# Kernel optimization log

Hardware: AMD Instinct MI355X
Metric: run time of the kernel (lower is better)

## Reference

```python
import jax, jax.numpy as jnp
import numpy as np

B = 4
IN_DIM = 512
HID = 1024
MLP_LAYERS = 2
SEQ = 4096          # output_dim / sequence_length
RH = 64             # ripl_hidden_dim
RL = 2              # ripl_num_layers
MULT = 1            # ripl_coordinate_multipler

MID_DIM = 2 * RH * RH + (RH + 1) * RH      # per middle ripple layer param count
OUT_DIM = 2 * RH * 1 + (RH + 1) * 1        # output ripple layer param count
MLP_OUT = RL * MID_DIM + OUT_DIM


def gelu(x):
    return jax.nn.gelu(x, approximate=False)


def layer_norm(x, g, b, eps=1e-5):
    mu = jnp.mean(x, axis=-1, keepdims=True)
    var = jnp.var(x, axis=-1, keepdims=True)
    return (x - mu) * jax.lax.rsqrt(var + eps) * g + b


def batch_ripple(x, w, b):
    # x: (B,S,I), w: (B,O,I,2), b: (B,O,I+1)
    # out[b,s,o] = b[b,o,0] + sum_i b[b,o,i+1] * sin(w[b,o,i,0]*x[b,s,i] + w[b,o,i,1])
    arg = w[:, None, :, :, 0] * x[:, :, None, :] + w[:, None, :, :, 1]  # (B,S,O,I)
    return b[:, None, :, 0] + jnp.sum(jnp.sin(arg) * b[:, None, :, 1:], axis=-1)


def setup_inputs() -> dict:
    key = jax.random.key(0)
    ks = jax.random.split(key, 20)
    s = 0.02
    inp = {
        "x": jax.random.normal(ks[0], (B, IN_DIM), jnp.float32),
        "mlp_w0": jax.random.normal(ks[1], (IN_DIM, HID), jnp.float32) * s,
        "mlp_b0": jnp.zeros((HID,), jnp.float32),
        "mlp_w1": jax.random.normal(ks[2], (HID, HID), jnp.float32) * s,
        "mlp_b1": jnp.zeros((HID,), jnp.float32),
        "ln_g1": jnp.ones((HID,), jnp.float32),
        "ln_b1": jnp.zeros((HID,), jnp.float32),
        "mlp_w2": jax.random.normal(ks[3], (HID, HID), jnp.float32) * s,
        "mlp_b2": jnp.zeros((HID,), jnp.float32),
        "ln_g2": jnp.ones((HID,), jnp.float32),
        "ln_b2": jnp.zeros((HID,), jnp.float32),
        "mlp_w3": jax.random.normal(ks[4], (HID, MLP_OUT), jnp.float32) * s,
        "mlp_b3": jnp.zeros((MLP_OUT,), jnp.float32),
        "lc_w": jax.random.normal(ks[5], (1, RH), jnp.float32) * 0.1,
        "lc_b": jax.random.normal(ks[6], (RH,), jnp.float32) * 0.1,
        "byp_w": jax.random.normal(ks[7], (1, 1, 2), jnp.float32),
        "byp_b": jax.random.normal(ks[8], (1, 2), jnp.float32),
    }
    return inp


def reference(x, mlp_w0, mlp_b0, mlp_w1, mlp_b1, ln_g1, ln_b1,
              mlp_w2, mlp_b2, ln_g2, ln_b2, mlp_w3, mlp_b3,
              lc_w, lc_b, byp_w, byp_b):
    # hypernetwork MLP: Linear+GELU, [Linear+LN+GELU]*2, Linear
    h = gelu(x @ mlp_w0 + mlp_b0)
    h = gelu(layer_norm(h @ mlp_w1 + mlp_b1, ln_g1, ln_b1))
    h = gelu(layer_norm(h @ mlp_w2 + mlp_b2, ln_g2, ln_b2))
    mlp_out = h @ mlp_w3 + mlp_b3                      # (B, MLP_OUT)

    # split into RL middle ripple layers then the output layer
    middles = [mlp_out[:, i * MID_DIM:(i + 1) * MID_DIM] for i in range(RL)]
    out_w = mlp_out[:, RL * MID_DIM:RL * MID_DIM + OUT_DIM]

    # line coordinates -> fc layer
    lc = (jnp.arange(SEQ, dtype=jnp.float32) * MULT)[None, :, None]  # (1,S,1)
    lc = jnp.broadcast_to(lc, (x.shape[0], SEQ, 1))
    lc_x = lc @ lc_w + lc_b                                          # (B,S,RH)
    lc_bypass = lc_x

    for mw in middles:
        w = mw[:, :2 * RH * RH].reshape(-1, RH, RH, 2)
        b = mw[:, 2 * RH * RH:].reshape(-1, RH, RH + 1)
        lc_x = gelu(batch_ripple(lc_x, w, b))

    wo = out_w[:, :2 * RH].reshape(-1, 1, RH, 2)
    bo = out_w[:, 2 * RH:].reshape(-1, 1, RH + 1)
    lc_x = batch_ripple(lc_x, wo, bo)                                # (B,S,1)

    # learned RippleLinear(1,1) bypass, broadcast over features then reduced
    byp = byp_b[0, 0] + jnp.sum(
        jnp.sin(byp_w[0, 0, 0] * lc_bypass + byp_w[0, 0, 1]) * byp_b[0, 1],
        axis=-1, keepdims=True)
    lc_x = lc_x + byp
    return jnp.transpose(lc_x, (0, 2, 1))                            # (B,1,S)
```

## Files before the change

kernel.cpp:

```cpp
#include <hip/hip_runtime.h>
#include <hip/hip_bf16.h>
#include <math.h>

#define B_      4
#define IN_DIM  512
#define HID     1024
#define SEQ     4096
#define RH      64
#define RL      2
#define MID_DIM 12352
#define OUT_DIM 193
#define MLP_OUT 24897
#define INV2PI  0.15915494309189535f

#define MLPT_STRIDE 25088

#define OFF_P0    0
#define OFF_P1    32768
#define OFF_H1    98304
#define OFF_P2    102400
#define OFF_H2    167936
#define OFF_P3    172032
#define OFF_MLPT  968736

__device__ __forceinline__ float gelu_exact(float v) {
    return 0.5f * v * (1.0f + erff(v * 0.70710678118654752f));
}

__device__ __forceinline__ float hw_sin_rev(float r) {
    r = r - __builtin_rintf(r);
    return __builtin_amdgcn_sinf(r);
}

__global__ void k_gemm0(const float* __restrict__ x, const float* __restrict__ w0,
                        float* __restrict__ p0) {
    const int cch = blockIdx.x;
    const int kc  = blockIdx.y;
    const int tid = threadIdx.x;
    __shared__ float xs[256];
    {
        const int b = tid >> 6, k = tid & 63;
        xs[tid] = x[b * IN_DIM + kc * 64 + k];
    }
    __syncthreads();
    const int b = tid >> 6, cl = tid & 63;
    const int c = cch * 64 + cl;
    const float* wp = w0 + (size_t)(kc * 64) * HID + c;
    const float* xp = xs + b * 64;
    float acc = 0.f;
    #pragma unroll 8
    for (int k = 0; k < 64; ++k)
        acc = fmaf(xp[k], wp[(size_t)k * HID], acc);
    p0[(kc * 4 + b) * HID + c] = acc;
}

__global__ void k_gemm1(const float* __restrict__ p0, const float* __restrict__ b0,
                        const float* __restrict__ w1, float* __restrict__ p1) {
    const int cch = blockIdx.x;
    const int kc  = blockIdx.y;
    const int tid = threadIdx.x;
    __shared__ float hs[256];
    {
        const int b = tid >> 6, k = tid & 63;
        const int kg = kc * 64 + k;
        float v = b0[kg];
        #pragma unroll
        for (int j = 0; j < 8; ++j) v += p0[(j * 4 + b) * HID + kg];
        hs[tid] = gelu_exact(v);
    }
    __syncthreads();
    const int b = tid >> 6, cl = tid & 63;
    const int c = cch * 64 + cl;
    const float* wp = w1 + (size_t)(kc * 64) * HID + c;
    const float* hp = hs + b * 64;
    float acc = 0.f;
    #pragma unroll 8
    for (int k = 0; k < 64; ++k)
        acc = fmaf(hp[k], wp[(size_t)k * HID], acc);
    p1[(kc * 4 + b) * HID + c] = acc;
}

__global__ void k_gemm2(const float* __restrict__ h, const float* __restrict__ w,
                        float* __restrict__ pout) {
    const int cch = blockIdx.x;
    const int kc  = blockIdx.y;
    const int tid = threadIdx.x;
    __shared__ float hs[256];
    {
        const int b = tid >> 6, k = tid & 63;
        hs[tid] = h[b * HID + kc * 64 + k];
    }
    __syncthreads();
    const int b = tid >> 6, cl = tid & 63;
    const int c = cch * 64 + cl;
    const float* wp = w + (size_t)(kc * 64) * HID + c;
    const float* hp = hs + b * 64;
    float acc = 0.f;
    #pragma unroll 8
    for (int k = 0; k < 64; ++k)
        acc = fmaf(hp[k], wp[(size_t)k * HID], acc);
    pout[(kc * 4 + b) * HID + c] = acc;
}

__global__ void k_lng(const float* __restrict__ part, const float* __restrict__ bias,
                      const float* __restrict__ g, const float* __restrict__ bl,
                      float* __restrict__ h) {
    const int b = blockIdx.x, tid = threadIdx.x;
    float v = bias[tid];
    #pragma unroll
    for (int j = 0; j < 16; ++j) v += part[(j * 4 + b) * HID + tid];
    float s1 = v, s2 = v * v;
    #pragma unroll
    for (int m = 1; m < 64; m <<= 1) {
        s1 += __shfl_xor(s1, m, 64);
        s2 += __shfl_xor(s2, m, 64);
    }
    __shared__ float r1[16], r2[16], s_mu, s_rs;
    const int lane = tid & 63, wid = tid >> 6;
    if (lane == 0) { r1[wid] = s1; r2[wid] = s2; }
    __syncthreads();
    if (tid == 0) {
        float a = 0.f, c = 0.f;
        #pragma unroll
        for (int j = 0; j < 16; ++j) { a += r1[j]; c += r2[j]; }
        const float mu = a * (1.0f / HID);
        s_mu = mu;
        s_rs = rsqrtf(c * (1.0f / HID) - mu * mu + 1e-5f);
    }
    __syncthreads();
    h[b * HID + tid] = gelu_exact((v - s_mu) * s_rs * g[tid] + bl[tid]);
}

__global__ void k_gemm3(const float* __restrict__ h2, const float* __restrict__ w3,
                        float* __restrict__ p3) {
    const int cch = blockIdx.x;
    const int kc  = blockIdx.y;
    const int tid = threadIdx.x;
    __shared__ float hs[512];
    for (int e = tid; e < 512; e += 256) {
        const int b = e >> 7, k = e & 127;
        hs[e] = h2[b * HID + kc * 128 + k];
    }
    __syncthreads();
    const int c = cch * 256 + tid;
    if (c >= MLP_OUT) return;
    const float* wp = w3 + (size_t)(kc * 128) * MLP_OUT + c;
    float a0 = 0.f, a1 = 0.f, a2 = 0.f, a3 = 0.f;
    #pragma unroll 16
    for (int k = 0; k < 128; ++k) {
        const float w = wp[(size_t)k * MLP_OUT];
        a0 = fmaf(hs[k],       w, a0);
        a1 = fmaf(hs[128 + k], w, a1);
        a2 = fmaf(hs[256 + k], w, a2);
        a3 = fmaf(hs[384 + k], w, a3);
    }
    p3[(size_t)(kc * 4 + 0) * MLP_OUT + c] = a0;
    p3[(size_t)(kc * 4 + 1) * MLP_OUT + c] = a1;
    p3[(size_t)(kc * 4 + 2) * MLP_OUT + c] = a2;
    p3[(size_t)(kc * 4 + 3) * MLP_OUT + c] = a3;
}

__global__ void k_comb3T(const float* __restrict__ p3, const float* __restrict__ b3,
                         float* __restrict__ mlpT) {
    const int d = blockIdx.x * 256 + threadIdx.x;
    const int b = blockIdx.y;
    int src = -1;
    float scale = 1.f;
    if (d < 24832) {
        const int l = d / 12416, r = d % 12416;
        const int base = l * MID_DIM;
        if (r < 8192) {
            const int half = r >> 12;
            const int rr = r & 4095;
            const int i = rr >> 6, o = rr & 63;
            src = base + o * 128 + i * 2 + half;
            scale = INV2PI;
        } else if (r < 12288) {
            const int rr = r - 8192;
            const int i = rr >> 6, o = rr & 63;
            src = base + 8192 + o * 65 + 1 + i;
        } else if (r < 12352) {
            const int o = r - 12288;
            src = base + 8192 + o * 65;
        }
    } else {
        const int rr = d - 24832;
        const int base = RL * MID_DIM;
        if (rr < 64)        { src = base + rr * 2;            scale = INV2PI; }
        else if (rr < 128)  { src = base + (rr - 64) * 2 + 1; scale = INV2PI; }
        else if (rr < 192)  { src = base + 128 + 1 + (rr - 128); }
        else if (rr == 192) { src = base + 128; }
    }
    float v = 0.f;
    if (src >= 0) {
        v = b3[src];
        #pragma unroll
        for (int j = 0; j < 8; ++j) v += p3[(size_t)(j * 4 + b) * MLP_OUT + src];
        v *= scale;
    }
    mlpT[(size_t)b * MLPT_STRIDE + d] = v;
}

__global__ void __launch_bounds__(256, 2) k_ripple(
        const float* __restrict__ mlpT, const float* __restrict__ lcw,
        const float* __restrict__ lcb, const float* __restrict__ bypw,
        const float* __restrict__ bypb, float* __restrict__ out) {
    const int tid = threadIdx.x;
    const int b = blockIdx.y;
    const int t0 = blockIdx.x * 32;
    const int lane = tid & 63, wid = tid >> 6, tb = wid * 8;

    __shared__ __align__(16) float s_w[12416];
    __shared__ __align__(16) float s_x[64 * 36];
    __shared__ __align__(16) float s_wo[256];
    __shared__ float s_red[32];

    const float* mb = mlpT + (size_t)b * MLPT_STRIDE;

    {
        const float4* src = reinterpret_cast<const float4*>(mb);
        float4* dst = reinterpret_cast<float4*>(s_w);
        for (int e = tid; e < 3104; e += 256) dst[e] = src[e];
        if (tid < 64) {
            reinterpret_cast<float4*>(s_wo)[tid] =
                reinterpret_cast<const float4*>(mb + 24832)[tid];
        }
    }
    const float lw = lcw[lane], lb = lcb[lane];
    for (int e = tid; e < 2048; e += 256) {
        const int i = e >> 5, tt = e & 31;
        s_x[i * 36 + tt] = fmaf((float)(t0 + tt), lcw[i], lcb[i]);
    }
    __syncthreads();

    float acc[8];
    for (int layer = 0; layer < 2; ++layer) {
        const float bc = s_w[12288 + lane];
        #pragma unroll
        for (int j = 0; j < 8; ++j) acc[j] = bc;
        for (int i = 0; i < 64; ++i) {
            const float ws = s_w[i * 64 + lane];
            const float wo = s_w[4096 + i * 64 + lane];
            const float bs = s_w[8192 + i * 64 + lane];
            const float4 xa = *reinterpret_cast<const float4*>(&s_x[i * 36 + tb]);
            const float4 xb = *reinterpret_cast<const float4*>(&s_x[i * 36 + tb + 4]);
            const float xv[8] = {xa.x, xa.y, xa.z, xa.w, xb.x, xb.y, xb.z, xb.w};
            #pragma unroll
            for (int j = 0; j < 8; ++j) {
                const float r = fmaf(ws, xv[j], wo);
                acc[j] = fmaf(hw_sin_rev(r), bs, acc[j]);
            }
        }
        __syncthreads();
        if (layer == 0) {
            #pragma unroll
            for (int j = 0; j < 8; ++j)
                s_x[lane * 36 + tb + j] = gelu_exact(acc[j]);
            const float4* src = reinterpret_cast<const float4*>(mb + 12416);
            float4* dst = reinterpret_cast<float4*>(s_w);
            for (int e = tid; e < 3104; e += 256) dst[e] = src[e];
            __syncthreads();
        }
    }

    {
        const float wsO = s_wo[lane], woO = s_wo[64 + lane], bsO = s_wo[128 + lane];
        const float bcO = s_wo[192];
        const float bw0 = bypw[0] * INV2PI, bw1 = bypw[1] * INV2PI;
        const float bb0 = bypb[0], bb1 = bypb[1];
        #pragma unroll
        for (int j = 0; j < 8; ++j) {
            const int t = t0 + tb + j;
            const float v = gelu_exact(acc[j]);
            float s = hw_sin_rev(fmaf(wsO, v, woO)) * bsO;
            const float xb = fmaf((float)t, lw, lb);
            s = fmaf(hw_sin_rev(fmaf(bw0, xb, bw1)), bb1, s);
            #pragma unroll
            for (int m = 1; m < 64; m <<= 1) s += __shfl_xor(s, m, 64);
            if (lane == 0) s_red[tb + j] = s + bcO + bb0;
        }
    }
    __syncthreads();
    if (tid < 32) out[(size_t)b * SEQ + t0 + tid] = s_red[tid];
}

extern "C" void kernel_launch(void* const* d_in, const int* in_sizes, int n_in,
                              void* d_out, int out_size, void* d_ws, size_t ws_size,
                              hipStream_t stream) {
    const float* x     = (const float*)d_in[0];
    const float* w0    = (const float*)d_in[1];
    const float* b0    = (const float*)d_in[2];
    const float* w1    = (const float*)d_in[3];
    const float* b1    = (const float*)d_in[4];
    const float* g1    = (const float*)d_in[5];
    const float* bln1  = (const float*)d_in[6];
    const float* w2    = (const float*)d_in[7];
    const float* b2    = (const float*)d_in[8];
    const float* g2    = (const float*)d_in[9];
    const float* bln2  = (const float*)d_in[10];
    const float* w3    = (const float*)d_in[11];
    const float* b3    = (const float*)d_in[12];
    const float* lcw   = (const float*)d_in[13];
    const float* lcb   = (const float*)d_in[14];
    const float* bypw  = (const float*)d_in[15];
    const float* bypb  = (const float*)d_in[16];
    float* out = (float*)d_out;
    float* ws  = (float*)d_ws;

    float* p0   = ws + OFF_P0;
    float* p1   = ws + OFF_P1;
    float* h1   = ws + OFF_H1;
    float* p2   = ws + OFF_P2;
    float* h2   = ws + OFF_H2;
    float* p3   = ws + OFF_P3;
    float* mlpT = ws + OFF_MLPT;

    k_gemm0 <<<dim3(16, 8),  256, 0, stream>>>(x,  w0, p0);
    k_gemm1 <<<dim3(16, 16), 256, 0, stream>>>(p0, b0, w1, p1);
    k_lng   <<<B_, 1024,     0, stream>>>(p1, b1, g1, bln1, h1);
    k_gemm2 <<<dim3(16, 16), 256, 0, stream>>>(h1, w2, p2);
    k_lng   <<<B_, 1024,     0, stream>>>(p2, b2, g2, bln2, h2);
    k_gemm3 <<<dim3(98, 8),  256, 0, stream>>>(h2, w3, p3);
    k_comb3T<<<dim3(98, B_), 256, 0, stream>>>(p3, b3, mlpT);
    k_ripple<<<dim3(SEQ / 32, B_), 256, 0, stream>>>(mlpT, lcw, lcb, bypw, bypb, out);
}
```

Before: 253.5 us.

## Fuse all MLP and ripple stages into one cooperative persistent kernel

Replaces eight separate launches with a single cooperative kernel that runs each stage as a grid-strided task loop separated by grid-wide syncs. The layer-norm kernels are folded into the following GEMM stages, with each block recomputing the per-row statistics redundantly. GEMM3 is re-split into fewer, longer K chunks, which halves the partial sums combined afterwards. This targets launch gaps and the tiny under-occupied LN launches, at the cost of grid.sync overhead, redundant LN work in every block, and host-side device and occupancy queries on every call.

```diff
diff --git a/kernel.cpp b/kernel.cpp
--- a/kernel.cpp
+++ b/kernel.cpp
@@ -1,15 +1,14 @@
 #include <hip/hip_runtime.h>
-#include <hip/hip_bf16.h>
+#include <hip/hip_cooperative_groups.h>
 #include <math.h>
+
+namespace cg = cooperative_groups;
 
 #define B_      4
 #define IN_DIM  512
 #define HID     1024
 #define SEQ     4096
-#define RH      64
-#define RL      2
 #define MID_DIM 12352
-#define OUT_DIM 193
 #define MLP_OUT 24897
 #define INV2PI  0.15915494309189535f
 
@@ -17,11 +16,9 @@
 
 #define OFF_P0    0
 #define OFF_P1    32768
-#define OFF_H1    98304
-#define OFF_P2    102400
-#define OFF_H2    167936
-#define OFF_P3    172032
-#define OFF_MLPT  968736
+#define OFF_P2    98304
+#define OFF_P3    163840
+#define OFF_MLPT  562192
 
 __device__ __forceinline__ float gelu_exact(float v) {
     return 0.5f * v * (1.0f + erff(v * 0.70710678118654752f));
@@ -32,295 +29,339 @@
     return __builtin_amdgcn_sinf(r);
 }
 
-__global__ void k_gemm0(const float* __restrict__ x, const float* __restrict__ w0,
-                        float* __restrict__ p0) {
-    const int cch = blockIdx.x;
-    const int kc  = blockIdx.y;
+__global__ void __launch_bounds__(256, 2) k_mega(
+    const float* __restrict__ x,  const float* __restrict__ w0, const float* __restrict__ b0,
+    const float* __restrict__ w1, const float* __restrict__ b1, const float* __restrict__ g1,
+    const float* __restrict__ bl1,
+    const float* __restrict__ w2, const float* __restrict__ b2, const float* __restrict__ g2,
+    const float* __restrict__ bl2,
+    const float* __restrict__ w3, const float* __restrict__ b3,
+    const float* __restrict__ lcw, const float* __restrict__ lcb,
+    const float* __restrict__ bypw, const float* __restrict__ bypb,
+    float* __restrict__ out, float* __restrict__ ws)
+{
+    cg::grid_group grid = cg::this_grid();
     const int tid = threadIdx.x;
-    __shared__ float xs[256];
-    {
-        const int b = tid >> 6, k = tid & 63;
-        xs[tid] = x[b * IN_DIM + kc * 64 + k];
-    }
-    __syncthreads();
-    const int b = tid >> 6, cl = tid & 63;
-    const int c = cch * 64 + cl;
-    const float* wp = w0 + (size_t)(kc * 64) * HID + c;
-    const float* xp = xs + b * 64;
-    float acc = 0.f;
-    #pragma unroll 8
-    for (int k = 0; k < 64; ++k)
-        acc = fmaf(xp[k], wp[(size_t)k * HID], acc);
-    p0[(kc * 4 + b) * HID + c] = acc;
-}
-
-__global__ void k_gemm1(const float* __restrict__ p0, const float* __restrict__ b0,
-                        const float* __restrict__ w1, float* __restrict__ p1) {
-    const int cch = blockIdx.x;
-    const int kc  = blockIdx.y;
-    const int tid = threadIdx.x;
-    __shared__ float hs[256];
-    {
-        const int b = tid >> 6, k = tid & 63;
-        const int kg = kc * 64 + k;
-        float v = b0[kg];
-        #pragma unroll
-        for (int j = 0; j < 8; ++j) v += p0[(j * 4 + b) * HID + kg];
-        hs[tid] = gelu_exact(v);
-    }
-    __syncthreads();
-    const int b = tid >> 6, cl = tid & 63;
-    const int c = cch * 64 + cl;
-    const float* wp = w1 + (size_t)(kc * 64) * HID + c;
-    const float* hp = hs + b * 64;
-    float acc = 0.f;
-    #pragma unroll 8
-    for (int k = 0; k < 64; ++k)
-        acc = fmaf(hp[k], wp[(size_t)k * HID], acc);
-    p1[(kc * 4 + b) * HID + c] = acc;
-}
-
-__global__ void k_gemm2(const float* __restrict__ h, const float* __restrict__ w,
-                        float* __restrict__ pout) {
-    const int cch = blockIdx.x;
-    const int kc  = blockIdx.y;
-    const int tid = threadIdx.x;
-    __shared__ float hs[256];
-    {
-        const int b = tid >> 6, k = tid & 63;
-        hs[tid] = h[b * HID + kc * 64 + k];
-    }
-    __syncthreads();
-    const int b = tid >> 6, cl = tid & 63;
-    const int c = cch * 64 + cl;
-    const float* wp = w + (size_t)(kc * 64) * HID + c;
-    const float* hp = hs + b * 64;
-    float acc = 0.f;
-    #pragma unroll 8
-    for (int k = 0; k < 64; ++k)
-        acc = fmaf(hp[k], wp[(size_t)k * HID], acc);
-    pout[(kc * 4 + b) * HID + c] = acc;
-}
-
-__global__ void k_lng(const float* __restrict__ part, const float* __restrict__ bias,
-                      const float* __restrict__ g, const float* __restrict__ bl,
-                      float* __restrict__ h) {
-    const int b = blockIdx.x, tid = threadIdx.x;
-    float v = bias[tid];
-    #pragma unroll
-    for (int j = 0; j < 16; ++j) v += part[(j * 4 + b) * HID + tid];
-    float s1 = v, s2 = v * v;
-    #pragma unroll
-    for (int m = 1; m < 64; m <<= 1) {
-        s1 += __shfl_xor(s1, m, 64);
-        s2 += __shfl_xor(s2, m, 64);
-    }
-    __shared__ float r1[16], r2[16], s_mu, s_rs;
-    const int lane = tid & 63, wid = tid >> 6;
-    if (lane == 0) { r1[wid] = s1; r2[wid] = s2; }
-    __syncthreads();
-    if (tid == 0) {
-        float a = 0.f, c = 0.f;
-        #pragma unroll
-        for (int j = 0; j < 16; ++j) { a += r1[j]; c += r2[j]; }
-        const float mu = a * (1.0f / HID);
-        s_mu = mu;
-        s_rs = rsqrtf(c * (1.0f / HID) - mu * mu + 1e-5f);
-    }
-    __syncthreads();
-    h[b * HID + tid] = gelu_exact((v - s_mu) * s_rs * g[tid] + bl[tid]);
-}
-
-__global__ void k_gemm3(const float* __restrict__ h2, const float* __restrict__ w3,
-                        float* __restrict__ p3) {
-    const int cch = blockIdx.x;
-    const int kc  = blockIdx.y;
-    const int tid = threadIdx.x;
-    __shared__ float hs[512];
-    for (int e = tid; e < 512; e += 256) {
-        const int b = e >> 7, k = e & 127;
-        hs[e] = h2[b * HID + kc * 128 + k];
-    }
-    __syncthreads();
-    const int c = cch * 256 + tid;
-    if (c >= MLP_OUT) return;
-    const float* wp = w3 + (size_t)(kc * 128) * MLP_OUT + c;
-    float a0 = 0.f, a1 = 0.f, a2 = 0.f, a3 = 0.f;
-    #pragma unroll 16
-    for (int k = 0; k < 128; ++k) {
-        const float w = wp[(size_t)k * MLP_OUT];
-        a0 = fmaf(hs[k],       w, a0);
-        a1 = fmaf(hs[128 + k], w, a1);
-        a2 = fmaf(hs[256 + k], w, a2);
-        a3 = fmaf(hs[384 + k], w, a3);
-    }
-    p3[(size_t)(kc * 4 + 0) * MLP_OUT + c] = a0;
-    p3[(size_t)(kc * 4 + 1) * MLP_OUT + c] = a1;
-    p3[(size_t)(kc * 4 + 2) * MLP_OUT + c] = a2;
-    p3[(size_t)(kc * 4 + 3) * MLP_OUT + c] = a3;
-}
-
-__global__ void k_comb3T(const float* __restrict__ p3, const float* __restrict__ b3,
-                         float* __restrict__ mlpT) {
-    const int d = blockIdx.x * 256 + threadIdx.x;
-    const int b = blockIdx.y;
-    int src = -1;
-    float scale = 1.f;
-    if (d < 24832) {
-        const int l = d / 12416, r = d % 12416;
-        const int base = l * MID_DIM;
-        if (r < 8192) {
-            const int half = r >> 12;
-            const int rr = r & 4095;
-            const int i = rr >> 6, o = rr & 63;
-            src = base + o * 128 + i * 2 + half;
-            scale = INV2PI;
-        } else if (r < 12288) {
-            const int rr = r - 8192;
-            const int i = rr >> 6, o = rr & 63;
-            src = base + 8192 + o * 65 + 1 + i;
-        } else if (r < 12352) {
-            const int o = r - 12288;
-            src = base + 8192 + o * 65;
-        }
-    } else {
-        const int rr = d - 24832;
-        const int base = RL * MID_DIM;
-        if (rr < 64)        { src = base + rr * 2;            scale = INV2PI; }
-        else if (rr < 128)  { src = base + (rr - 64) * 2 + 1; scale = INV2PI; }
-        else if (rr < 192)  { src = base + 128 + 1 + (rr - 128); }
-        else if (rr == 192) { src = base + 128; }
-    }
-    float v = 0.f;
-    if (src >= 0) {
-        v = b3[src];
-        #pragma unroll
-        for (int j = 0; j < 8; ++j) v += p3[(size_t)(j * 4 + b) * MLP_OUT + src];
-        v *= scale;
-    }
-    mlpT[(size_t)b * MLPT_STRIDE + d] = v;
-}
-
-__global__ void __launch_bounds__(256, 2) k_ripple(
-        const float* __restrict__ mlpT, const float* __restrict__ lcw,
-        const float* __restrict__ lcb, const float* __restrict__ bypw,
-        const float* __restrict__ bypb, float* __restrict__ out) {
-    const int tid = threadIdx.x;
-    const int b = blockIdx.y;
-    const int t0 = blockIdx.x * 32;
-    const int lane = tid & 63, wid = tid >> 6, tb = wid * 8;
+    const int nblk = gridDim.x;
+
+    float* p0   = ws + OFF_P0;
+    float* p1   = ws + OFF_P1;
+    float* p2   = ws + OFF_P2;
+    float* p3   = ws + OFF_P3;
+    float* mlpT = ws + OFF_MLPT;
 
     __shared__ __align__(16) float s_w[12416];
-    __shared__ __align__(16) float s_x[64 * 36];
+    __shared__ __align__(16) float s_x[2304];
     __shared__ __align__(16) float s_wo[256];
-    __shared__ float s_red[32];
-
-    const float* mb = mlpT + (size_t)b * MLPT_STRIDE;
-
-    {
-        const float4* src = reinterpret_cast<const float4*>(mb);
-        float4* dst = reinterpret_cast<float4*>(s_w);
-        for (int e = tid; e < 3104; e += 256) dst[e] = src[e];
-        if (tid < 64) {
-            reinterpret_cast<float4*>(s_wo)[tid] =
-                reinterpret_cast<const float4*>(mb + 24832)[tid];
-        }
-    }
-    const float lw = lcw[lane], lb = lcb[lane];
-    for (int e = tid; e < 2048; e += 256) {
-        const int i = e >> 5, tt = e & 31;
-        s_x[i * 36 + tt] = fmaf((float)(t0 + tt), lcw[i], lcb[i]);
-    }
-    __syncthreads();
-
-    float acc[8];
-    for (int layer = 0; layer < 2; ++layer) {
-        const float bc = s_w[12288 + lane];
-        #pragma unroll
-        for (int j = 0; j < 8; ++j) acc[j] = bc;
-        for (int i = 0; i < 64; ++i) {
-            const float ws = s_w[i * 64 + lane];
-            const float wo = s_w[4096 + i * 64 + lane];
-            const float bs = s_w[8192 + i * 64 + lane];
-            const float4 xa = *reinterpret_cast<const float4*>(&s_x[i * 36 + tb]);
-            const float4 xb = *reinterpret_cast<const float4*>(&s_x[i * 36 + tb + 4]);
-            const float xv[8] = {xa.x, xa.y, xa.z, xa.w, xb.x, xb.y, xb.z, xb.w};
-            #pragma unroll
-            for (int j = 0; j < 8; ++j) {
-                const float r = fmaf(ws, xv[j], wo);
-                acc[j] = fmaf(hw_sin_rev(r), bs, acc[j]);
-            }
-        }
-        __syncthreads();
-        if (layer == 0) {
-            #pragma unroll
-            for (int j = 0; j < 8; ++j)
-                s_x[lane * 36 + tb + j] = gelu_exact(acc[j]);
-            const float4* src = reinterpret_cast<const float4*>(mb + 12416);
+    __shared__ float s_red[64];
+    __shared__ float s_hs[256];
+
+    for (int task = blockIdx.x; task < 128; task += nblk) {
+        const int cch = task >> 3, kc = task & 7;
+        {
+            const int b = tid >> 6, k = tid & 63;
+            s_hs[tid] = x[b * IN_DIM + kc * 64 + k];
+        }
+        __syncthreads();
+        const int b = tid >> 6, cl = tid & 63;
+        const int c = cch * 64 + cl;
+        const float* wp = w0 + (size_t)(kc * 64) * HID + c;
+        const float* xp = s_hs + b * 64;
+        float acc = 0.f;
+        #pragma unroll 8
+        for (int k = 0; k < 64; ++k) acc = fmaf(xp[k], wp[(size_t)k * HID], acc);
+        p0[(kc * 4 + b) * HID + c] = acc;
+        __syncthreads();
+    }
+    grid.sync();
+
+    for (int task = blockIdx.x; task < 256; task += nblk) {
+        const int cch = task >> 4, kc = task & 15;
+        {
+            const int b = tid >> 6, k = tid & 63;
+            const int kg = kc * 64 + k;
+            float v = b0[kg];
+            #pragma unroll
+            for (int j = 0; j < 8; ++j) v += p0[(j * 4 + b) * HID + kg];
+            s_hs[tid] = gelu_exact(v);
+        }
+        __syncthreads();
+        const int b = tid >> 6, cl = tid & 63;
+        const int c = cch * 64 + cl;
+        const float* wp = w1 + (size_t)(kc * 64) * HID + c;
+        const float* hp = s_hs + b * 64;
+        float acc = 0.f;
+        #pragma unroll 8
+        for (int k = 0; k < 64; ++k) acc = fmaf(hp[k], wp[(size_t)k * HID], acc);
+        p1[(kc * 4 + b) * HID + c] = acc;
+        __syncthreads();
+    }
+    grid.sync();
+
+    for (int task = blockIdx.x; task < 256; task += nblk) {
+        const int cch = task >> 4, kc = task & 15;
+        float* vbuf = s_w;
+        for (int e = tid; e < 4096; e += 256) {
+            const int b = e >> 10, c = e & 1023;
+            float v = b1[c];
+            #pragma unroll
+            for (int j = 0; j < 16; ++j) v += p1[(j * 4 + b) * HID + c];
+            vbuf[e] = v;
+        }
+        __syncthreads();
+        {
+            const int b = tid >> 6, lane = tid & 63;
+            float s1 = 0.f, s2 = 0.f;
+            #pragma unroll
+            for (int j = 0; j < 16; ++j) {
+                const float v = vbuf[b * 1024 + lane + 64 * j];
+                s1 += v; s2 += v * v;
+            }
+            #pragma unroll
+            for (int m = 1; m < 64; m <<= 1) {
+                s1 += __shfl_xor(s1, m, 64);
+                s2 += __shfl_xor(s2, m, 64);
+            }
+            if (lane == 0) {
+                const float mu = s1 * (1.0f / HID);
+                s_red[b] = mu;
+                s_red[4 + b] = rsqrtf(s2 * (1.0f / HID) - mu * mu + 1e-5f);
+            }
+        }
+        __syncthreads();
+        {
+            const int b = tid >> 6, kl = tid & 63;
+            const int c = kc * 64 + kl;
+            const float v = vbuf[b * 1024 + c];
+            s_hs[tid] = gelu_exact((v - s_red[b]) * s_red[4 + b] * g1[c] + bl1[c]);
+        }
+        __syncthreads();
+        const int b = tid >> 6, cl = tid & 63;
+        const int c = cch * 64 + cl;
+        const float* wp = w2 + (size_t)(kc * 64) * HID + c;
+        const float* hp = s_hs + b * 64;
+        float acc = 0.f;
+        #pragma unroll 8
+        for (int k = 0; k < 64; ++k) acc = fmaf(hp[k], wp[(size_t)k * HID], acc);
+        p2[(kc * 4 + b) * HID + c] = acc;
+        __syncthreads();
+    }
+    grid.sync();
+
+    for (int task = blockIdx.x; task < 392; task += nblk) {
+        const int cch = task >> 2, kc = task & 3;
+        float* vbuf = s_w;
+        for (int e = tid; e < 4096; e += 256) {
+            const int b = e >> 10, c = e & 1023;
+            float v = b2[c];
+            #pragma unroll
+            for (int j = 0; j < 16; ++j) v += p2[(j * 4 + b) * HID + c];
+            vbuf[e] = v;
+        }
+        __syncthreads();
+        {
+            const int b = tid >> 6, lane = tid & 63;
+            float s1 = 0.f, s2 = 0.f;
+            #pragma unroll
+            for (int j = 0; j < 16; ++j) {
+                const float v = vbuf[b * 1024 + lane + 64 * j];
+                s1 += v; s2 += v * v;
+            }
+            #pragma unroll
+            for (int m = 1; m < 64; m <<= 1) {
+                s1 += __shfl_xor(s1, m, 64);
+                s2 += __shfl_xor(s2, m, 64);
+            }
+            if (lane == 0) {
+                const float mu = s1 * (1.0f / HID);
+                s_red[b] = mu;
+                s_red[4 + b] = rsqrtf(s2 * (1.0f / HID) - mu * mu + 1e-5f);
+            }
+        }
+        __syncthreads();
+        for (int e = tid; e < 4096; e += 256) {
+            const int b = e >> 10, c = e & 1023;
+            vbuf[e] = gelu_exact((vbuf[e] - s_red[b]) * s_red[4 + b] * g2[c] + bl2[c]);
+        }
+        __syncthreads();
+        const int c = cch * 256 + tid;
+        if (c < MLP_OUT) {
+            const float* wp = w3 + (size_t)(kc * 256) * MLP_OUT + c;
+            const float* h0p = vbuf + kc * 256;
+            float a0 = 0.f, a1 = 0.f, a2 = 0.f, a3 = 0.f;
+            #pragma unroll 16
+            for (int k = 0; k < 256; ++k) {
+                const float w = wp[(size_t)k * MLP_OUT];
+                a0 = fmaf(h0p[k],        w, a0);
+                a1 = fmaf(h0p[1024 + k], w, a1);
+                a2 = fmaf(h0p[2048 + k], w, a2);
+                a3 = fmaf(h0p[3072 + k], w, a3);
+            }
+            p3[(size_t)(kc * 4 + 0) * MLP_OUT + c] = a0;
+            p3[(size_t)(kc * 4 + 1) * MLP_OUT + c] = a1;
+            p3[(size_t)(kc * 4 + 2) * MLP_OUT + c] = a2;
+            p3[(size_t)(kc * 4 + 3) * MLP_OUT + c] = a3;
+        }
+        __syncthreads();
+    }
+    grid.sync();
+
+    for (int task = blockIdx.x; task < 392; task += nblk) {
+        const int cch = task >> 2, b = task & 3;
+        const int d = cch * 256 + tid;
+        if (d < MLPT_STRIDE) {
+            int src = -1;
+            float scale = 1.f;
+            if (d < 24832) {
+                const int l = d / 12416, r = d % 12416;
+                const int base = l * MID_DIM;
+                if (r < 8192) {
+                    const int half = r >> 12;
+                    const int rr = r & 4095;
+                    const int i = rr >> 6, o = rr & 63;
+                    src = base + o * 128 + i * 2 + half;
+                    scale = INV2PI;
+                } else if (r < 12288) {
+                    const int rr = r - 8192;
+                    const int i = rr >> 6, o = rr & 63;
+                    src = base + 8192 + o * 65 + 1 + i;
+                } else if (r < 12352) {
+                    src = base + 8192 + (r - 12288) * 65;
+                }
+            } else {
+                const int rr = d - 24832;
+                const int base = 2 * MID_DIM;
+                if (rr < 64)        { src = base + rr * 2;            scale = INV2PI; }
+                else if (rr < 128)  { src = base + (rr - 64) * 2 + 1; scale = INV2PI; }
+                else if (rr < 192)  { src = base + 128 + 1 + (rr - 128); }
+                else if (rr == 192) { src = base + 128; }
+            }
+            float v = 0.f;
+            if (src >= 0) {
+                v = b3[src];
+                #pragma unroll
+                for (int j = 0; j < 4; ++j) v += p3[(size_t)(j * 4 + b) * MLP_OUT + src];
+                v *= scale;
+            }
+            mlpT[(size_t)b * MLPT_STRIDE + d] = v;
+        }
+    }
+    grid.sync();
+
+    for (int task = blockIdx.x; task < 512; task += nblk) {
+        const int b = task >> 7;
+        const int t0 = (task & 127) * 32;
+        const int lane = tid & 63, wid = tid >> 6, tb = wid * 8;
+        const float* mb = mlpT + (size_t)b * MLPT_STRIDE;
+
+        {
+            const float4* src = reinterpret_cast<const float4*>(mb);
             float4* dst = reinterpret_cast<float4*>(s_w);
             for (int e = tid; e < 3104; e += 256) dst[e] = src[e];
+            if (tid < 64)
+                reinterpret_cast<float4*>(s_wo)[tid] =
+                    reinterpret_cast<const float4*>(mb + 24832)[tid];
+        }
+        const float lw = lcw[lane], lb = lcb[lane];
+        for (int e = tid; e < 2048; e += 256) {
+            const int i = e >> 5, tt = e & 31;
+            s_x[i * 36 + tt] = fmaf((float)(t0 + tt), lcw[i], lcb[i]);
+        }
+        __syncthreads();
+
+        float acc[8];
+        for (int layer = 0; layer < 2; ++layer) {
+            const float bc = s_w[12288 + lane];
+            #pragma unroll
+            for (int j = 0; j < 8; ++j) acc[j] = bc;
+            for (int i = 0; i < 64; ++i) {
+                const float wsv = s_w[i * 64 + lane];
+                const float wov = s_w[4096 + i * 64 + lane];
+                const float bsv = s_w[8192 + i * 64 + lane];
+                const float4 xa = *reinterpret_cast<const float4*>(&s_x[i * 36 + tb]);
+                const float4 xb = *reinterpret_cast<const float4*>(&s_x[i * 36 + tb + 4]);
+                const float xv[8] = {xa.x, xa.y, xa.z, xa.w, xb.x, xb.y, xb.z, xb.w};
+                #pragma unroll
+                for (int j = 0; j < 8; ++j) {
+                    const float r = fmaf(wsv, xv[j], wov);
+                    acc[j] = fmaf(hw_sin_rev(r), bsv, acc[j]);
+                }
+            }
             __syncthreads();
-        }
-    }
-
-    {
-        const float wsO = s_wo[lane], woO = s_wo[64 + lane], bsO = s_wo[128 + lane];
-        const float bcO = s_wo[192];
-        const float bw0 = bypw[0] * INV2PI, bw1 = bypw[1] * INV2PI;
-        const float bb0 = bypb[0], bb1 = bypb[1];
-        #pragma unroll
-        for (int j = 0; j < 8; ++j) {
-            const int t = t0 + tb + j;
-            const float v = gelu_exact(acc[j]);
-            float s = hw_sin_rev(fmaf(wsO, v, woO)) * bsO;
-            const float xb = fmaf((float)t, lw, lb);
-            s = fmaf(hw_sin_rev(fmaf(bw0, xb, bw1)), bb1, s);
-            #pragma unroll
-            for (int m = 1; m < 64; m <<= 1) s += __shfl_xor(s, m, 64);
-            if (lane == 0) s_red[tb + j] = s + bcO + bb0;
-        }
-    }
-    __syncthreads();
-    if (tid < 32) out[(size_t)b * SEQ + t0 + tid] = s_red[tid];
+            if (layer == 0) {
+                #pragma unroll
+                for (int j = 0; j < 8; ++j)
+                    s_x[lane * 36 + tb + j] = gelu_exact(acc[j]);
+                const float4* src = reinterpret_cast<const float4*>(mb + 12416);
+                float4* dst = reinterpret_cast<float4*>(s_w);
+                for (int e = tid; e < 3104; e += 256) dst[e] = src[e];
+                __syncthreads();
+            }
+        }
+
+        {
+            const float wsO = s_wo[lane], woO = s_wo[64 + lane], bsO = s_wo[128 + lane];
+            const float bcO = s_wo[192];
+            const float bw0 = bypw[0] * INV2PI, bw1 = bypw[1] * INV2PI;
+            const float bb0 = bypb[0], bb1 = bypb[1];
+            #pragma unroll
+            for (int j = 0; j < 8; ++j) {
+                const int t = t0 + tb + j;
+                const float v = gelu_exact(acc[j]);
+                float s = hw_sin_rev(fmaf(wsO, v, woO)) * bsO;
+                const float xb = fmaf((float)t, lw, lb);
+                s = fmaf(hw_sin_rev(fmaf(bw0, xb, bw1)), bb1, s);
+                #pragma unroll
+                for (int m = 1; m < 64; m <<= 1) s += __shfl_xor(s, m, 64);
+                if (lane == 0) s_red[tb + j] = s + bcO + bb0;
+            }
+        }
+        __syncthreads();
+        if (tid < 32) out[(size_t)b * SEQ + t0 + tid] = s_red[tid];
+        __syncthreads();
+    }
 }
 
 extern "C" void kernel_launch(void* const* d_in, const int* in_sizes, int n_in,
                               void* d_out, int out_size, void* d_ws, size_t ws_size,
                               hipStream_t stream) {
-    const float* x     = (const float*)d_in[0];
-    const float* w0    = (const float*)d_in[1];
-    const float* b0    = (const float*)d_in[2];
-    const float* w1    = (const float*)d_in[3];
-    const float* b1    = (const float*)d_in[4];
-    const float* g1    = (const float*)d_in[5];
-    const float* bln1  = (const float*)d_in[6];
-    const float* w2    = (const float*)d_in[7];
-    const float* b2    = (const float*)d_in[8];
-    const float* g2    = (const float*)d_in[9];
-    const float* bln2  = (const float*)d_in[10];
-    const float* w3    = (const float*)d_in[11];
-    const float* b3    = (const float*)d_in[12];
-    const float* lcw   = (const float*)d_in[13];
-    const float* lcb   = (const float*)d_in[14];
-    const float* bypw  = (const float*)d_in[15];
-    const float* bypb  = (const float*)d_in[16];
+    const float* x    = (const float*)d_in[0];
+    const float* w0   = (const float*)d_in[1];
+    const float* b0   = (const float*)d_in[2];
+    const float* w1   = (const float*)d_in[3];
+    const float* b1   = (const float*)d_in[4];
+    const float* g1   = (const float*)d_in[5];
+    const float* bl1  = (const float*)d_in[6];
+    const float* w2   = (const float*)d_in[7];
+    const float* b2   = (const float*)d_in[8];
+    const float* g2   = (const float*)d_in[9];
+    const float* bl2  = (const float*)d_in[10];
+    const float* w3   = (const float*)d_in[11];
+    const float* b3   = (const float*)d_in[12];
+    const float* lcw  = (const float*)d_in[13];
+    const float* lcb  = (const float*)d_in[14];
+    const float* bypw = (const float*)d_in[15];
+    const float* bypb = (const float*)d_in[16];
     float* out = (float*)d_out;
     float* ws  = (float*)d_ws;
 
-    float* p0   = ws + OFF_P0;
-    float* p1   = ws + OFF_P1;
-    float* h1   = ws + OFF_H1;
-    float* p2   = ws + OFF_P2;
-    float* h2   = ws + OFF_H2;
-    float* p3   = ws + OFF_P3;
-    float* mlpT = ws + OFF_MLPT;
-
-    k_gemm0 <<<dim3(16, 8),  256, 0, stream>>>(x,  w0, p0);
-    k_gemm1 <<<dim3(16, 16), 256, 0, stream>>>(p0, b0, w1, p1);
-    k_lng   <<<B_, 1024,     0, stream>>>(p1, b1, g1, bln1, h1);
-    k_gemm2 <<<dim3(16, 16), 256, 0, stream>>>(h1, w2, p2);
-    k_lng   <<<B_, 1024,     0, stream>>>(p2, b2, g2, bln2, h2);
-    k_gemm3 <<<dim3(98, 8),  256, 0, stream>>>(h2, w3, p3);
-    k_comb3T<<<dim3(98, B_), 256, 0, stream>>>(p3, b3, mlpT);
-    k_ripple<<<dim3(SEQ / 32, B_), 256, 0, stream>>>(mlpT, lcw, lcb, bypw, bypb, out);
+    int dev = 0;
+    hipGetDevice(&dev);
+    hipDeviceProp_t prop;
+    hipGetDeviceProperties(&prop, dev);
+    int occ = 0;
+    hipOccupancyMaxActiveBlocksPerMultiprocessor(&occ, k_mega, 256, 0);
+    int grid = occ * prop.multiProcessorCount;
+    if (grid > 512) grid = 512;
+    if (grid < 1)  grid = 1;
+
+    void* args[] = {
+        (void*)&x,  (void*)&w0, (void*)&b0,
+        (void*)&w1, (void*)&b1, (void*)&g1, (void*)&bl1,
+        (void*)&w2, (void*)&b2, (void*)&g2, (void*)&bl2,
+        (void*)&w3, (void*)&b3, (void*)&lcw, (void*)&lcb,
+        (void*)&bypw, (void*)&bypb, (void*)&out, (void*)&ws
+    };
+    hipLaunchCooperativeKernel((const void*)k_mega, dim3(grid), dim3(256),
+                               args, 0, stream);
 }
```

Result: slower. 575.7 us (+127.1%).

## Fuse first layernorm into gemm2 and merge gemm3 with transpose epilogue

Applied to the files above, without the earlier changes.

Removes the first layernorm kernel by having every gemm2 block recompute the row statistics from the partial sums. gemm1/gemm2 switch to a 256-wide K split with fewer partials. gemm3 now does the full K=1024 reduction per output column and writes the permuted, scaled mlpT layout directly, which drops the p3 partial buffer and the comb3T kernel. The intent is fewer launches and less intermediate traffic, at the cost of redundant layernorm work per block and longer serial K loops with fewer blocks in flight.

```diff
diff --git a/kernel.cpp b/kernel.cpp
--- a/kernel.cpp
+++ b/kernel.cpp
@@ -1,15 +1,11 @@
 #include <hip/hip_runtime.h>
-#include <hip/hip_bf16.h>
 #include <math.h>
 
 #define B_      4
 #define IN_DIM  512
 #define HID     1024
 #define SEQ     4096
-#define RH      64
-#define RL      2
 #define MID_DIM 12352
-#define OUT_DIM 193
 #define MLP_OUT 24897
 #define INV2PI  0.15915494309189535f
 
@@ -17,11 +13,9 @@
 
 #define OFF_P0    0
 #define OFF_P1    32768
-#define OFF_H1    98304
-#define OFF_P2    102400
-#define OFF_H2    167936
-#define OFF_P3    172032
-#define OFF_MLPT  968736
+#define OFF_P2    49152
+#define OFF_H2    65536
+#define OFF_MLPT  69632
 
 __device__ __forceinline__ float gelu_exact(float v) {
     return 0.5f * v * (1.0f + erff(v * 0.70710678118654752f));
@@ -34,8 +28,7 @@
 
 __global__ void k_gemm0(const float* __restrict__ x, const float* __restrict__ w0,
                         float* __restrict__ p0) {
-    const int cch = blockIdx.x;
-    const int kc  = blockIdx.y;
+    const int cch = blockIdx.x, kc = blockIdx.y;
     const int tid = threadIdx.x;
     __shared__ float xs[256];
     {
@@ -48,67 +41,95 @@
     const float* wp = w0 + (size_t)(kc * 64) * HID + c;
     const float* xp = xs + b * 64;
     float acc = 0.f;
-    #pragma unroll 8
-    for (int k = 0; k < 64; ++k)
-        acc = fmaf(xp[k], wp[(size_t)k * HID], acc);
+    #pragma unroll 16
+    for (int k = 0; k < 64; ++k) acc = fmaf(xp[k], wp[(size_t)k * HID], acc);
     p0[(kc * 4 + b) * HID + c] = acc;
 }
 
 __global__ void k_gemm1(const float* __restrict__ p0, const float* __restrict__ b0,
                         const float* __restrict__ w1, float* __restrict__ p1) {
-    const int cch = blockIdx.x;
-    const int kc  = blockIdx.y;
-    const int tid = threadIdx.x;
-    __shared__ float hs[256];
-    {
-        const int b = tid >> 6, k = tid & 63;
-        const int kg = kc * 64 + k;
+    const int cch = blockIdx.x, kc = blockIdx.y;
+    const int tid = threadIdx.x;
+    __shared__ float s_h[1024];
+    for (int e = tid; e < 1024; e += 256) {
+        const int b = e >> 8, kk = e & 255;
+        const int kg = kc * 256 + kk;
         float v = b0[kg];
         #pragma unroll
         for (int j = 0; j < 8; ++j) v += p0[(j * 4 + b) * HID + kg];
-        hs[tid] = gelu_exact(v);
+        s_h[e] = gelu_exact(v);
     }
     __syncthreads();
     const int b = tid >> 6, cl = tid & 63;
     const int c = cch * 64 + cl;
-    const float* wp = w1 + (size_t)(kc * 64) * HID + c;
-    const float* hp = hs + b * 64;
+    const float* wp = w1 + (size_t)(kc * 256) * HID + c;
+    const float* hp = s_h + b * 256;
     float acc = 0.f;
-    #pragma unroll 8
-    for (int k = 0; k < 64; ++k)
-        acc = fmaf(hp[k], wp[(size_t)k * HID], acc);
+    #pragma unroll 16
+    for (int k = 0; k < 256; ++k) acc = fmaf(hp[k], wp[(size_t)k * HID], acc);
     p1[(kc * 4 + b) * HID + c] = acc;
 }
 
-__global__ void k_gemm2(const float* __restrict__ h, const float* __restrict__ w,
-                        float* __restrict__ pout) {
-    const int cch = blockIdx.x;
-    const int kc  = blockIdx.y;
-    const int tid = threadIdx.x;
-    __shared__ float hs[256];
+__global__ void k_gemm2(const float* __restrict__ p1, const float* __restrict__ b1,
+                        const float* __restrict__ g1, const float* __restrict__ bl1,
+                        const float* __restrict__ w2, float* __restrict__ p2) {
+    const int cch = blockIdx.x, kc = blockIdx.y;
+    const int tid = threadIdx.x;
+    __shared__ __align__(16) float vbuf[4096];
+    __shared__ float s_h[1024];
+    __shared__ float s_red[8];
+    for (int e = tid; e < 4096; e += 256) {
+        const int b = e >> 10, c = e & 1023;
+        float v = b1[c];
+        #pragma unroll
+        for (int j = 0; j < 4; ++j) v += p1[(j * 4 + b) * HID + c];
+        vbuf[e] = v;
+    }
+    __syncthreads();
     {
-        const int b = tid >> 6, k = tid & 63;
-        hs[tid] = h[b * HID + kc * 64 + k];
+        const int b = tid >> 6, lane = tid & 63;
+        float s1 = 0.f, s2 = 0.f;
+        #pragma unroll
+        for (int jj = 0; jj < 16; ++jj) {
+            const float v = vbuf[b * 1024 + lane + 64 * jj];
+            s1 += v; s2 += v * v;
+        }
+        #pragma unroll
+        for (int m = 1; m < 64; m <<= 1) {
+            s1 += __shfl_xor(s1, m, 64);
+            s2 += __shfl_xor(s2, m, 64);
+        }
+        if (lane == 0) {
+            const float mu = s1 * (1.0f / HID);
+            s_red[b] = mu;
+            s_red[4 + b] = rsqrtf(s2 * (1.0f / HID) - mu * mu + 1e-5f);
+        }
+    }
+    __syncthreads();
+    for (int e = tid; e < 1024; e += 256) {
+        const int b = e >> 8, kk = e & 255;
+        const int c = kc * 256 + kk;
+        const float v = vbuf[b * 1024 + c];
+        s_h[e] = gelu_exact((v - s_red[b]) * s_red[4 + b] * g1[c] + bl1[c]);
     }
     __syncthreads();
     const int b = tid >> 6, cl = tid & 63;
     const int c = cch * 64 + cl;
-    const float* wp = w + (size_t)(kc * 64) * HID + c;
-    const float* hp = hs + b * 64;
+    const float* wp = w2 + (size_t)(kc * 256) * HID + c;
+    const float* hp = s_h + b * 256;
     float acc = 0.f;
-    #pragma unroll 8
-    for (int k = 0; k < 64; ++k)
-        acc = fmaf(hp[k], wp[(size_t)k * HID], acc);
-    pout[(kc * 4 + b) * HID + c] = acc;
-}
-
-__global__ void k_lng(const float* __restrict__ part, const float* __restrict__ bias,
-                      const float* __restrict__ g, const float* __restrict__ bl,
-                      float* __restrict__ h) {
+    #pragma unroll 16
+    for (int k = 0; k < 256; ++k) acc = fmaf(hp[k], wp[(size_t)k * HID], acc);
+    p2[(kc * 4 + b) * HID + c] = acc;
+}
+
+__global__ void k_lng2(const float* __restrict__ p2, const float* __restrict__ b2,
+                       const float* __restrict__ g2, const float* __restrict__ bl2,
+                       float* __restrict__ h2) {
     const int b = blockIdx.x, tid = threadIdx.x;
-    float v = bias[tid];
+    float v = b2[tid];
     #pragma unroll
-    for (int j = 0; j < 16; ++j) v += part[(j * 4 + b) * HID + tid];
+    for (int j = 0; j < 4; ++j) v += p2[(j * 4 + b) * HID + tid];
     float s1 = v, s2 = v * v;
     #pragma unroll
     for (int m = 1; m < 64; m <<= 1) {
@@ -128,77 +149,46 @@
         s_rs = rsqrtf(c * (1.0f / HID) - mu * mu + 1e-5f);
     }
     __syncthreads();
-    h[b * HID + tid] = gelu_exact((v - s_mu) * s_rs * g[tid] + bl[tid]);
-}
-
-__global__ void k_gemm3(const float* __restrict__ h2, const float* __restrict__ w3,
-                        float* __restrict__ p3) {
-    const int cch = blockIdx.x;
-    const int kc  = blockIdx.y;
-    const int tid = threadIdx.x;
-    __shared__ float hs[512];
-    for (int e = tid; e < 512; e += 256) {
-        const int b = e >> 7, k = e & 127;
-        hs[e] = h2[b * HID + kc * 128 + k];
-    }
-    __syncthreads();
-    const int c = cch * 256 + tid;
-    if (c >= MLP_OUT) return;
-    const float* wp = w3 + (size_t)(kc * 128) * MLP_OUT + c;
-    float a0 = 0.f, a1 = 0.f, a2 = 0.f, a3 = 0.f;
+    h2[b * HID + tid] = gelu_exact((v - s_mu) * s_rs * g2[tid] + bl2[tid]);
+}
+
+__global__ void k_gemm3T(const float* __restrict__ h2, const float* __restrict__ w3,
+                         const float* __restrict__ b3, float* __restrict__ mlpT) {
+    const int tid = threadIdx.x;
+    const int cl = tid & 63;
+    const int bu = __builtin_amdgcn_readfirstlane(tid >> 6);
+    const int c_raw = blockIdx.x * 64 + cl;
+    const bool valid = c_raw < MLP_OUT;
+    const int c = valid ? c_raw : (MLP_OUT - 1);
+    const float* hp = h2 + bu * HID;
+    const float* wp = w3 + c;
+    float acc = 0.f;
     #pragma unroll 16
-    for (int k = 0; k < 128; ++k) {
-        const float w = wp[(size_t)k * MLP_OUT];
-        a0 = fmaf(hs[k],       w, a0);
-        a1 = fmaf(hs[128 + k], w, a1);
-        a2 = fmaf(hs[256 + k], w, a2);
-        a3 = fmaf(hs[384 + k], w, a3);
-    }
-    p3[(size_t)(kc * 4 + 0) * MLP_OUT + c] = a0;
-    p3[(size_t)(kc * 4 + 1) * MLP_OUT + c] = a1;
-    p3[(size_t)(kc * 4 + 2) * MLP_OUT + c] = a2;
-    p3[(size_t)(kc * 4 + 3) * MLP_OUT + c] = a3;
-}
-
-__global__ void k_comb3T(const float* __restrict__ p3, const float* __restrict__ b3,
-                         float* __restrict__ mlpT) {
-    const int d = blockIdx.x * 256 + threadIdx.x;
-    const int b = blockIdx.y;
-    int src = -1;
-    float scale = 1.f;
-    if (d < 24832) {
-        const int l = d / 12416, r = d % 12416;
-        const int base = l * MID_DIM;
-        if (r < 8192) {
-            const int half = r >> 12;
-            const int rr = r & 4095;
-            const int i = rr >> 6, o = rr & 63;
-            src = base + o * 128 + i * 2 + half;
-            scale = INV2PI;
-        } else if (r < 12288) {
-            const int rr = r - 8192;
-            const int i = rr >> 6, o = rr & 63;
-            src = base + 8192 + o * 65 + 1 + i;
-        } else if (r < 12352) {
-            const int o = r - 12288;
-            src = base + 8192 + o * 65;
+    for (int k = 0; k < 1024; ++k)
+        acc = fmaf(hp[k], wp[(size_t)k * MLP_OUT], acc);
+    if (!valid) return;
+    const float v = acc + b3[c];
+    int d; float sc = 1.f;
+    if (c < 2 * MID_DIM) {
+        const int l = c / MID_DIM;
+        const int rel = c - l * MID_DIM;
+        if (rel < 8192) {
+            const int o = rel >> 7, low = rel & 127;
+            d = l * 12416 + (low & 1) * 4096 + (low >> 1) * 64 + o;
+            sc = INV2PI;
+        } else {
+            const int r2 = rel - 8192;
+            const int o = r2 / 65, j = r2 % 65;
+            d = (j == 0) ? (l * 12416 + 12288 + o)
+                         : (l * 12416 + 8192 + (j - 1) * 64 + o);
         }
     } else {
-        const int rr = d - 24832;
-        const int base = RL * MID_DIM;
-        if (rr < 64)        { src = base + rr * 2;            scale = INV2PI; }
-        else if (rr < 128)  { src = base + (rr - 64) * 2 + 1; scale = INV2PI; }
-        else if (rr < 192)  { src = base + 128 + 1 + (rr - 128); }
-        else if (rr == 192) { src = base + 128; }
-    }
-    float v = 0.f;
-    if (src >= 0) {
-        v = b3[src];
-        #pragma unroll
-        for (int j = 0; j < 8; ++j) v += p3[(size_t)(j * 4 + b) * MLP_OUT + src];
-        v *= scale;
-    }
-    mlpT[(size_t)b * MLPT_STRIDE + d] = v;
+        const int rel = c - 2 * MID_DIM;
+        if (rel < 128)       { d = 24832 + (rel & 1) * 64 + (rel >> 1); sc = INV2PI; }
+        else if (rel == 128) { d = 24832 + 192; }
+        else                 { d = 24832 + 128 + (rel - 129); }
+    }
+    mlpT[(size_t)bu * MLPT_STRIDE + d] = v * sc;
 }
 
 __global__ void __launch_bounds__(256, 2) k_ripple(
@@ -211,7 +201,7 @@
     const int lane = tid & 63, wid = tid >> 6, tb = wid * 8;
 
     __shared__ __align__(16) float s_w[12416];
-    __shared__ __align__(16) float s_x[64 * 36];
+    __shared__ __align__(16) float s_x[2304];
     __shared__ __align__(16) float s_wo[256];
     __shared__ float s_red[32];
 
@@ -221,10 +211,9 @@
         const float4* src = reinterpret_cast<const float4*>(mb);
         float4* dst = reinterpret_cast<float4*>(s_w);
         for (int e = tid; e < 3104; e += 256) dst[e] = src[e];
-        if (tid < 64) {
+        if (tid < 64)
             reinterpret_cast<float4*>(s_wo)[tid] =
                 reinterpret_cast<const float4*>(mb + 24832)[tid];
-        }
     }
     const float lw = lcw[lane], lb = lcb[lane];
     for (int e = tid; e < 2048; e += 256) {
@@ -239,16 +228,16 @@
         #pragma unroll
         for (int j = 0; j < 8; ++j) acc[j] = bc;
         for (int i = 0; i < 64; ++i) {
-            const float ws = s_w[i * 64 + lane];
-            const float wo = s_w[4096 + i * 64 + lane];
-            const float bs = s_w[8192 + i * 64 + lane];
+            const float wsv = s_w[i * 64 + lane];
+            const float wov = s_w[4096 + i * 64 + lane];
+            const float bsv = s_w[8192 + i * 64 + lane];
             const float4 xa = *reinterpret_cast<const float4*>(&s_x[i * 36 + tb]);
             const float4 xb = *reinterpret_cast<const float4*>(&s_x[i * 36 + tb + 4]);
             const float xv[8] = {xa.x, xa.y, xa.z, xa.w, xb.x, xb.y, xb.z, xb.w};
             #pragma unroll
             for (int j = 0; j < 8; ++j) {
-                const float r = fmaf(ws, xv[j], wo);
-                acc[j] = fmaf(hw_sin_rev(r), bs, acc[j]);
+                const float r = fmaf(wsv, xv[j], wov);
+                acc[j] = fmaf(hw_sin_rev(r), bsv, acc[j]);
             }
         }
         __syncthreads();
@@ -287,40 +276,36 @@
 extern "C" void kernel_launch(void* const* d_in, const int* in_sizes, int n_in,
                               void* d_out, int out_size, void* d_ws, size_t ws_size,
                               hipStream_t stream) {
-    const float* x     = (const float*)d_in[0];
-    const float* w0    = (const float*)d_in[1];
-    const float* b0    = (const float*)d_in[2];
-    const float* w1    = (const float*)d_in[3];
-    const float* b1    = (const float*)d_in[4];
-    const float* g1    = (const float*)d_in[5];
-    const float* bln1  = (const float*)d_in[6];
-    const float* w2    = (const float*)d_in[7];
-    const float* b2    = (const float*)d_in[8];
-    const float* g2    = (const float*)d_in[9];
-    const float* bln2  = (const float*)d_in[10];
-    const float* w3    = (const float*)d_in[11];
-    const float* b3    = (const float*)d_in[12];
-    const float* lcw   = (const float*)d_in[13];
-    const float* lcb   = (const float*)d_in[14];
-    const float* bypw  = (const float*)d_in[15];
-    const float* bypb  = (const float*)d_in[16];
+    const float* x    = (const float*)d_in[0];
+    const float* w0   = (const float*)d_in[1];
+    const float* b0   = (const float*)d_in[2];
+    const float* w1   = (const float*)d_in[3];
+    const float* b1   = (const float*)d_in[4];
+    const float* g1   = (const float*)d_in[5];
+    const float* bl1  = (const float*)d_in[6];
+    const float* w2   = (const float*)d_in[7];
+    const float* b2   = (const float*)d_in[8];
+    const float* g2   = (const float*)d_in[9];
+    const float* bl2  = (const float*)d_in[10];
+    const float* w3   = (const float*)d_in[11];
+    const float* b3   = (const float*)d_in[12];
+    const float* lcw  = (const float*)d_in[13];
+    const float* lcb  = (const float*)d_in[14];
+    const float* bypw = (const float*)d_in[15];
+    const float* bypb = (const float*)d_in[16];
     float* out = (float*)d_out;
     float* ws  = (float*)d_ws;
 
     float* p0   = ws + OFF_P0;
     float* p1   = ws + OFF_P1;
-    float* h1   = ws + OFF_H1;
     float* p2   = ws + OFF_P2;
     float* h2   = ws + OFF_H2;
-    float* p3   = ws + OFF_P3;
     float* mlpT = ws + OFF_MLPT;
 
-    k_gemm0 <<<dim3(16, 8),  256, 0, stream>>>(x,  w0, p0);
-    k_gemm1 <<<dim3(16, 16), 256, 0, stream>>>(p0, b0, w1, p1);
-    k_lng   <<<B_, 1024,     0, stream>>>(p1, b1, g1, bln1, h1);
-    k_gemm2 <<<dim3(16, 16), 256, 0, stream>>>(h1, w2, p2);
-    k_lng   <<<B_, 1024,     0, stream>>>(p2, b2, g2, bln2, h2);
-    k_gemm3 <<<dim3(98, 8),  256, 0, stream>>>(h2, w3, p3);
-    k_comb3T<<<dim3(98, B_), 256, 0, stream>>>(p3, b3, mlpT);
+    k_gemm0 <<<dim3(16, 8), 256, 0, stream>>>(x, w0, p0);
+    k_gemm1 <<<dim3(16, 4), 256, 0, stream>>>(p0, b0, w1, p1);
+    k_gemm2 <<<dim3(16, 4), 256, 0, stream>>>(p1, b1, g1, bl1, w2, p2);
+    k_lng2  <<<B_, 1024,    0, stream>>>(p2, b2, g2, bl2, h2);
+    k_gemm3T<<<390, 256,    0, stream>>>(h2, w3, b3, mlpT);
     k_ripple<<<dim3(SEQ / 32, B_), 256, 0, stream>>>(mlpT, lcw, lcb, bypw, bypb, out);
 }
```

New measurement: 282.4 us. 1.11x slower.
